# Performance work log

Hardware: AMD Instinct MI355X
Metric: run time of the kernel (lower is better)

The kernel has to match this reference:

```python
import jax, jax.numpy as jnp
import numpy as np

B, T, D = 4, 2048, 1024
H = 16
HD = D // H  # 64
SCALE = 1.0 / np.sqrt(HD).astype(np.float32)


def setup_inputs() -> dict:
    key = jax.random.key(0)
    ks = jax.random.split(key, 5)
    std = 0.02
    return {
        "x": jax.random.normal(ks[0], (B, T, D), dtype=jnp.float32),
        "wq": jax.random.normal(ks[1], (D, D), dtype=jnp.float32) * std,
        "wk": jax.random.normal(ks[2], (D, D), dtype=jnp.float32) * std,
        "wv": jax.random.normal(ks[3], (D, D), dtype=jnp.float32) * std,
        "wo": jax.random.normal(ks[4], (D, D), dtype=jnp.float32) * std,
    }


def _shape(t):
    # [B,T,D] -> [B,H,T,HD]
    Bt, Tt, _ = t.shape
    return t.reshape(Bt, Tt, H, HD).transpose(0, 2, 1, 3)


def reference(x, wq, wk, wv, wo):
    # Linear layers are y = x @ W^T (torch nn.Linear semantics, no bias)
    q = _shape(x @ wq.T)  # [B,H,T,HD]
    k = _shape(x @ wk.T)
    v = _shape(x @ wv.T)
    att = jnp.einsum("bhqd,bhkd->bhqk", q, k) * SCALE  # [B,H,T,T]
    # causal mask: -inf strictly above diagonal
    causal = jnp.triu(jnp.full((T, T), -jnp.inf, dtype=att.dtype), k=1)
    att = att + causal[None, None, :, :]
    att = jax.nn.softmax(att.astype(jnp.float32), axis=-1).astype(att.dtype)
    # dropout prob = 0.0 -> identity
    y = jnp.einsum("bhqk,bhkd->bhqd", att, v)  # [B,H,T,HD]
    y = y.transpose(0, 2, 1, 3).reshape(B, T, D)
    return y @ wo.T
```

## Files before the change

kernel.cpp:

```cpp
#include <hip/hip_runtime.h>
#include <hip/hip_bf16.h>

#define BB 4
#define TT 2048
#define DDIM 1024
#define HH 16
#define HD 64

typedef __bf16 bf16_t;
typedef __bf16 bf16x4 __attribute__((ext_vector_type(4)));
typedef __bf16 bf16x8 __attribute__((ext_vector_type(8)));
typedef float f32x4 __attribute__((ext_vector_type(4)));

#define GLOAD_LDS(gp, lp) \
    __builtin_amdgcn_global_load_lds( \
        (const __attribute__((address_space(1))) void*)(gp), \
        (__attribute__((address_space(3))) void*)(lp), 16, 0, 0)

__global__ __launch_bounds__(256) void cvt_f32_bf16(
    const float* __restrict__ src, bf16_t* __restrict__ dst, size_t n8)
{
    size_t i = (size_t)blockIdx.x * blockDim.x + threadIdx.x;
    const size_t stride = (size_t)gridDim.x * blockDim.x;
    for (; i < n8; i += stride) {
        const f32x4 a = ((const f32x4*)src)[2 * i];
        const f32x4 b = ((const f32x4*)src)[2 * i + 1];
        bf16x8 v;
#pragma unroll
        for (int j = 0; j < 4; j++) { v[j] = (bf16_t)a[j]; v[4 + j] = (bf16_t)b[j]; }
        ((bf16x8*)dst)[i] = v;
    }
}

__global__ __launch_bounds__(256) void cvt_wpack(
    const float* __restrict__ s0, const float* __restrict__ s1,
    const float* __restrict__ s2, const float* __restrict__ s3,
    bf16_t* __restrict__ dst)
{
    const size_t n8 = (size_t)4 * DDIM * DDIM / 8;
    size_t i = (size_t)blockIdx.x * blockDim.x + threadIdx.x;
    const size_t stride = (size_t)gridDim.x * blockDim.x;
    for (; i < n8; i += stride) {
        const int sel = (int)(i >> 17);
        const float* s = sel == 0 ? s0 : sel == 1 ? s1 : sel == 2 ? s2 : s3;
        const size_t off8 = i & ((1u << 17) - 1);
        const f32x4 a = ((const f32x4*)s)[2 * off8];
        const f32x4 b = ((const f32x4*)s)[2 * off8 + 1];
        bf16x8 v;
#pragma unroll
        for (int j = 0; j < 4; j++) { v[j] = (bf16_t)a[j]; v[4 + j] = (bf16_t)b[j]; }
        ((bf16x8*)dst)[i] = v;
    }
}

__device__ __forceinline__ void stage8(const bf16_t* __restrict__ g, int ld,
                                       bf16_t* __restrict__ ldsbase, int lane)
{
    const int rr = lane >> 3;
    const int cc = (lane & 7) ^ ((rr & 1) << 2);
    GLOAD_LDS(&g[(size_t)rr * ld + cc * 8], ldsbase);
}

__global__ __launch_bounds__(256) void gemm_qkv(
    const bf16_t* __restrict__ A, const bf16_t* __restrict__ Wqkv,
    bf16_t* __restrict__ Qo, bf16_t* __restrict__ Ko, bf16_t* __restrict__ Vto,
    int M, int K)
{
    __shared__ alignas(16) bf16_t As[128 * 64];
    __shared__ alignas(16) bf16_t Bs[128 * 64];

    const int tid  = threadIdx.x;
    const int lane = tid & 63;
    const int w    = tid >> 6;
    const int quad = lane >> 4;
    const int l15  = lane & 15;
    const int wm   = (w >> 1) * 64;
    const int wn   = (w & 1) * 64;

    const int nwg = gridDim.x * gridDim.y;
    const int cpx = nwg >> 3;
    int id = blockIdx.y * gridDim.x + blockIdx.x;
    id = (id & 7) * cpx + (id >> 3);
    const int tileN = (id % 24) * 128;
    const int tileM = (id / 24) * 128;

    const f32x4 vzero = {0.f, 0.f, 0.f, 0.f};
    f32x4 acc[4][4];
#pragma unroll
    for (int i = 0; i < 4; i++)
#pragma unroll
        for (int j = 0; j < 4; j++) acc[i][j] = vzero;

    const int par4 = (l15 & 1) << 2;

    for (int k0 = 0; k0 < K; k0 += 64) {
        __syncthreads();
#pragma unroll
        for (int q = 0; q < 4; q++) {
            const int r0 = w * 32 + q * 8;
            stage8(&A[(size_t)(tileM + r0) * K + k0], K, &As[r0 * 64], lane);
            stage8(&Wqkv[(size_t)(tileN + r0) * K + k0], K, &Bs[r0 * 64], lane);
        }
        __syncthreads();

#pragma unroll
        for (int ss = 0; ss < 2; ss++) {
            const int phys = ((ss * 4 + quad) ^ par4) << 3;
            bf16x8 af[4], bf[4];
#pragma unroll
            for (int i = 0; i < 4; i++)
                af[i] = *(bf16x8*)&As[(wm + i * 16 + l15) * 64 + phys];
#pragma unroll
            for (int j = 0; j < 4; j++)
                bf[j] = *(bf16x8*)&Bs[(wn + j * 16 + l15) * 64 + phys];
#pragma unroll
            for (int i = 0; i < 4; i++)
#pragma unroll
                for (int j = 0; j < 4; j++)
                    acc[i][j] = __builtin_amdgcn_mfma_f32_16x16x32_bf16(
                        af[i], bf[j], acc[i][j], 0, 0, 0);
        }
    }

    const int region = tileN >> 10;
    const float osc = (region == 0) ? 0.125f * 1.44269504f : 1.0f;
#pragma unroll
    for (int i = 0; i < 4; i++) {
        const int row = tileM + wm + i * 16 + quad * 4;
#pragma unroll
        for (int j = 0; j < 4; j++) {
            const int ncol = tileN + wn + j * 16 + l15;
            if (region == 2) {
                const int cl = ncol - 2048;
                const int h = cl >> 6, d = cl & 63;
                const int bb = row >> 11, tloc = row & (TT - 1);
                bf16x4 pk;
#pragma unroll
                for (int r = 0; r < 4; r++) pk[r] = (bf16_t)acc[i][j][r];
                *(bf16x4*)&Vto[(((size_t)bb * HH + h) * HD + d) * TT + tloc] = pk;
            } else {
                bf16_t* dst = (region == 0) ? Qo : Ko;
                const int cl = ncol & 1023;
#pragma unroll
                for (int r = 0; r < 4; r++)
                    dst[(size_t)(row + r) * DDIM + cl] = (bf16_t)(acc[i][j][r] * osc);
            }
        }
    }
}

__global__ __launch_bounds__(256) void gemm_out(
    const bf16_t* __restrict__ A, const bf16_t* __restrict__ Bm,
    float* __restrict__ C, int M, int N, int K)
{
    __shared__ alignas(16) bf16_t As[128 * 64];
    __shared__ alignas(16) bf16_t Bs[128 * 64];

    const int tid  = threadIdx.x;
    const int lane = tid & 63;
    const int w    = tid >> 6;
    const int quad = lane >> 4;
    const int l15  = lane & 15;
    const int wm   = (w >> 1) * 64;
    const int wn   = (w & 1) * 64;

    const int nwg = gridDim.x * gridDim.y;
    const int cpx = nwg >> 3;
    int id = blockIdx.y * gridDim.x + blockIdx.x;
    id = (id & 7) * cpx + (id >> 3);
    const int tileN = (id % 8) * 128;
    const int tileM = (id / 8) * 128;

    const f32x4 vzero = {0.f, 0.f, 0.f, 0.f};
    f32x4 acc[4][4];
#pragma unroll
    for (int i = 0; i < 4; i++)
#pragma unroll
        for (int j = 0; j < 4; j++) acc[i][j] = vzero;

    const int par4 = (l15 & 1) << 2;

    for (int k0 = 0; k0 < K; k0 += 64) {
        __syncthreads();
#pragma unroll
        for (int q = 0; q < 4; q++) {
            const int r0 = w * 32 + q * 8;
            stage8(&A[(size_t)(tileM + r0) * K + k0], K, &As[r0 * 64], lane);
            stage8(&Bm[(size_t)(tileN + r0) * K + k0], K, &Bs[r0 * 64], lane);
        }
        __syncthreads();

#pragma unroll
        for (int ss = 0; ss < 2; ss++) {
            const int phys = ((ss * 4 + quad) ^ par4) << 3;
            bf16x8 af[4], bf[4];
#pragma unroll
            for (int i = 0; i < 4; i++)
                af[i] = *(bf16x8*)&As[(wm + i * 16 + l15) * 64 + phys];
#pragma unroll
            for (int j = 0; j < 4; j++)
                bf[j] = *(bf16x8*)&Bs[(wn + j * 16 + l15) * 64 + phys];
#pragma unroll
            for (int i = 0; i < 4; i++)
#pragma unroll
                for (int j = 0; j < 4; j++)
                    acc[i][j] = __builtin_amdgcn_mfma_f32_16x16x32_bf16(
                        af[i], bf[j], acc[i][j], 0, 0, 0);
        }
    }

#pragma unroll
    for (int i = 0; i < 4; i++) {
#pragma unroll
        for (int r = 0; r < 4; r++) {
            const int row = tileM + wm + i * 16 + quad * 4 + r;
#pragma unroll
            for (int j = 0; j < 4; j++)
                C[(size_t)row * N + tileN + wn + j * 16 + l15] = acc[i][j][r];
        }
    }
}

__global__ __launch_bounds__(256, 2) void attn_causal(
    const bf16_t* __restrict__ Q, const bf16_t* __restrict__ Kg,
    const bf16_t* __restrict__ Vt_g, bf16_t* __restrict__ Y)
{
    __shared__ alignas(16) bf16_t Ks[2 * 64 * 72];
    __shared__ alignas(16) bf16_t Vt[2 * 64 * 72];
    __shared__ alignas(16) bf16_t Ps[4][32 * 72];

    const int tid  = threadIdx.x;
    const int lane = tid & 63;
    const int w    = tid >> 6;
    const int quad = lane >> 4;
    const int l15  = lane & 15;
    const int bh   = blockIdx.x;
    const int sp   = blockIdx.y;
    const int b = bh >> 4, h = bh & 15;

    const int stg_row = tid >> 3;
    const int stg_c8  = (tid & 7) * 8;
    const int stg_off = stg_row * 72 + stg_c8;

    const f32x4 vzero = {0.f, 0.f, 0.f, 0.f};
    bf16x8 ones;
#pragma unroll
    for (int j = 0; j < 8; j++) ones[j] = (l15 == 0) ? (bf16_t)1.0f : (bf16_t)0.0f;

    const bf16_t* kg0 = &Kg[(size_t)(b * TT + stg_row) * DDIM + h * 64 + stg_c8];
    const bf16_t* vg0 = &Vt_g[((size_t)bh * HD + stg_row) * TT + stg_c8];

#pragma unroll 1
    for (int half = 0; half < 2; half++) {
        const int strip = half ? (15 - sp) : sp;
        const int qbase = strip * 128;

        bf16x8 qf[2][2];
#pragma unroll
        for (int mi = 0; mi < 2; mi++) {
            const size_t rq =
                (size_t)(b * TT + qbase + w * 32 + mi * 16 + l15) * DDIM + h * 64;
            qf[mi][0] = *(const bf16x8*)&Q[rq + quad * 8];
            qf[mi][1] = *(const bf16x8*)&Q[rq + 32 + quad * 8];
        }

        f32x4 o[2][4], o4[2];
#pragma unroll
        for (int mi = 0; mi < 2; mi++) {
#pragma unroll
            for (int c = 0; c < 4; c++) o[mi][c] = vzero;
            o4[mi] = vzero;
        }

        const int nkt = 2 * strip + 2;

        bf16x8 kreg[2], vreg[2];
#pragma unroll
        for (int p = 0; p < 2; p++) {
            kreg[p] = *(const bf16x8*)&kg0[(size_t)(p * 32) * DDIM];
            vreg[p] = *(const bf16x8*)&vg0[(size_t)(p * 32) * TT];
        }

#pragma unroll 1
        for (int kt = 0; kt < nkt; kt++) {
            const int kbase = kt * 64;
            const int coff = (kt & 1) * (64 * 72);
#pragma unroll
            for (int p = 0; p < 2; p++) {
                *(bf16x8*)&Ks[coff + stg_off + p * 32 * 72] = kreg[p];
                *(bf16x8*)&Vt[coff + stg_off + p * 32 * 72] = vreg[p];
            }
            if (kt + 1 < nkt) {
                const int nb = (kt + 1) * 64;
#pragma unroll
                for (int p = 0; p < 2; p++) {
                    kreg[p] = *(const bf16x8*)&kg0[(size_t)(nb + p * 32) * DDIM];
                    vreg[p] = *(const bf16x8*)&vg0[(size_t)(p * 32) * TT + nb];
                }
            }
            __syncthreads();

            f32x4 s[2][4];
            __builtin_amdgcn_s_setprio(1);
#pragma unroll
            for (int c = 0; c < 4; c++) {
                bf16x8 kf0 = *(bf16x8*)&Ks[coff + (c * 16 + l15) * 72 + quad * 8];
                bf16x8 kf1 = *(bf16x8*)&Ks[coff + (c * 16 + l15) * 72 + 32 + quad * 8];
#pragma unroll
                for (int mi = 0; mi < 2; mi++) {
                    f32x4 t = __builtin_amdgcn_mfma_f32_16x16x32_bf16(
                        qf[mi][0], kf0, vzero, 0, 0, 0);
                    s[mi][c] = __builtin_amdgcn_mfma_f32_16x16x32_bf16(
                        qf[mi][1], kf1, t, 0, 0, 0);
                }
            }
            __builtin_amdgcn_s_setprio(0);

#pragma unroll
            for (int mi = 0; mi < 2; mi++) {
                const int qlow = qbase + w * 32 + mi * 16;
                const bool need = (kbase + 63 > qlow);
#pragma unroll
                for (int r = 0; r < 4; r++) {
                    const int qrow = qlow + quad * 4 + r;
                    const int prow = mi * 16 + quad * 4 + r;
#pragma unroll
                    for (int c = 0; c < 4; c++) {
                        float sv = s[mi][c][r];
                        if (need && (kbase + c * 16 + l15 > qrow)) sv = -1e30f;
                        const int pchunk = (c * 2 + (l15 >> 3)) ^ (prow >> 2);
                        Ps[w][prow * 72 + (pchunk << 3) + (l15 & 7)] =
                            (bf16_t)__builtin_amdgcn_exp2f(sv);
                    }
                }
            }

            __builtin_amdgcn_s_setprio(1);
#pragma unroll
            for (int ss = 0; ss < 2; ss++) {
                bf16x8 pf[2];
#pragma unroll
                for (int mi = 0; mi < 2; mi++) {
                    const int m = mi * 16 + l15;
                    pf[mi] = *(bf16x8*)&Ps[w][m * 72 +
                                              ((((ss * 4 + quad) ^ (m >> 2)) & 7) << 3)];
                }
#pragma unroll
                for (int c = 0; c < 4; c++) {
                    bf16x8 vf = *(bf16x8*)&Vt[coff + (c * 16 + l15) * 72 + ss * 32 + quad * 8];
#pragma unroll
                    for (int mi = 0; mi < 2; mi++)
                        o[mi][c] = __builtin_amdgcn_mfma_f32_16x16x32_bf16(
                            pf[mi], vf, o[mi][c], 0, 0, 0);
                }
#pragma unroll
                for (int mi = 0; mi < 2; mi++)
                    o4[mi] = __builtin_amdgcn_mfma_f32_16x16x32_bf16(
                        pf[mi], ones, o4[mi], 0, 0, 0);
            }
            __builtin_amdgcn_s_setprio(0);
        }

#pragma unroll
        for (int mi = 0; mi < 2; mi++) {
#pragma unroll
            for (int r = 0; r < 4; r++) {
                const float lsum = __shfl(o4[mi][r], lane & 48, 64);
                const float inv = 1.0f / lsum;
                const int q = qbase + w * 32 + mi * 16 + quad * 4 + r;
#pragma unroll
                for (int c = 0; c < 4; c++)
                    Y[(size_t)(b * TT + q) * DDIM + h * 64 + c * 16 + l15] =
                        (bf16_t)(o[mi][c][r] * inv);
            }
        }
    }
}

extern "C" void kernel_launch(void* const* d_in, const int* in_sizes, int n_in,
                              void* d_out, int out_size, void* d_ws, size_t ws_size,
                              hipStream_t stream) {
    (void)in_sizes; (void)n_in; (void)out_size;
    const float* x  = (const float*)d_in[0];
    float* out = (float*)d_out;

    const int M = BB * TT;
    const size_t REGION = (size_t)M * DDIM;
    const size_t WREG   = (size_t)DDIM * DDIM;
    const size_t BATCH  = (size_t)TT * DDIM;
    bf16_t* ws = (bf16_t*)d_ws;

    if (ws_size >= (72ull << 20)) {
        bf16_t* xb  = ws;
        bf16_t* wpk = ws + REGION;
        bf16_t* Qb  = wpk + 4 * WREG;
        bf16_t* Kb  = Qb + REGION;
        bf16_t* Vtb = Kb + REGION;

        cvt_f32_bf16<<<1024, 256, 0, stream>>>(x, xb, REGION / 8);
        cvt_wpack<<<512, 256, 0, stream>>>(
            (const float*)d_in[1], (const float*)d_in[2],
            (const float*)d_in[3], (const float*)d_in[4], wpk);

        gemm_qkv<<<dim3(24, M / 128), 256, 0, stream>>>(
            xb, wpk, Qb, Kb, Vtb, M, DDIM);
        attn_causal<<<dim3(BB * HH, 8), 256, 0, stream>>>(Qb, Kb, Vtb, Qb);
        gemm_out<<<dim3(8, M / 128), 256, 0, stream>>>(
            Qb, wpk + 3 * WREG, out, M, DDIM, DDIM);
    } else {
        bf16_t* wpk = ws;
        bf16_t* xbb = ws + 4 * WREG;
        bf16_t* Qb  = xbb + BATCH;
        bf16_t* Kb  = Qb + BATCH;
        bf16_t* Vtb = Kb + BATCH;

        cvt_wpack<<<512, 256, 0, stream>>>(
            (const float*)d_in[1], (const float*)d_in[2],
            (const float*)d_in[3], (const float*)d_in[4], wpk);

        for (int b = 0; b < BB; b++) {
            const float* x_b = x + (size_t)b * BATCH;
            float* out_b = out + (size_t)b * BATCH;
            cvt_f32_bf16<<<512, 256, 0, stream>>>(x_b, xbb, BATCH / 8);
            gemm_qkv<<<dim3(24, TT / 128), 256, 0, stream>>>(
                xbb, wpk, Qb, Kb, Vtb, TT, DDIM);
            attn_causal<<<dim3(HH, 8), 256, 0, stream>>>(Qb, Kb, Vtb, Qb);
            gemm_out<<<dim3(8, TT / 128), 256, 0, stream>>>(
                Qb, wpk + 3 * WREG, out_b, TT, DDIM, DDIM);
        }
    }
}
```

Before: 254.4 us.

## Double-buffer GEMM LDS tiles, widen XOR swizzle, and raise attention occupancy

Both projection GEMMs now use two LDS buffers, so the next K-tile's global-to-LDS copy is issued before the MFMAs on the current tile, with one barrier per iteration instead of two. MFMA blocks are wrapped in raised wave priority. The LDS swizzle changes from a 1-bit XOR to a full 3-bit row XOR in the GEMMs and in attention, where the padded 72-wide K/V tiles become unpadded 64-wide swizzled tiles. The saved LDS lets attention's launch bound ask for 3 blocks per CU, at the cost of register pressure and the GEMMs' doubled LDS footprint.

Result: faster. 244.8 us (-3.8%).

```diff
diff --git a/kernel.cpp b/kernel.cpp
--- a/kernel.cpp
+++ b/kernel.cpp
@@ -57,7 +57,7 @@
                                        bf16_t* __restrict__ ldsbase, int lane)
 {
     const int rr = lane >> 3;
-    const int cc = (lane & 7) ^ ((rr & 1) << 2);
+    const int cc = (lane & 7) ^ rr;
     GLOAD_LDS(&g[(size_t)rr * ld + cc * 8], ldsbase);
 }
 
@@ -66,8 +66,8 @@
     bf16_t* __restrict__ Qo, bf16_t* __restrict__ Ko, bf16_t* __restrict__ Vto,
     int M, int K)
 {
-    __shared__ alignas(16) bf16_t As[128 * 64];
-    __shared__ alignas(16) bf16_t Bs[128 * 64];
+    __shared__ alignas(16) bf16_t As[2][128 * 64];
+    __shared__ alignas(16) bf16_t Bs[2][128 * 64];
 
     const int tid  = threadIdx.x;
     const int lane = tid & 63;
@@ -91,35 +91,51 @@
 #pragma unroll
         for (int j = 0; j < 4; j++) acc[i][j] = vzero;
 
-    const int par4 = (l15 & 1) << 2;
-
-    for (int k0 = 0; k0 < K; k0 += 64) {
-        __syncthreads();
-#pragma unroll
-        for (int q = 0; q < 4; q++) {
-            const int r0 = w * 32 + q * 8;
-            stage8(&A[(size_t)(tileM + r0) * K + k0], K, &As[r0 * 64], lane);
-            stage8(&Wqkv[(size_t)(tileN + r0) * K + k0], K, &Bs[r0 * 64], lane);
-        }
-        __syncthreads();
+    const int par8 = l15 & 7;
+
+#pragma unroll
+    for (int q = 0; q < 4; q++) {
+        const int r0 = w * 32 + q * 8;
+        stage8(&A[(size_t)(tileM + r0) * K], K, &As[0][r0 * 64], lane);
+        stage8(&Wqkv[(size_t)(tileN + r0) * K], K, &Bs[0][r0 * 64], lane);
+    }
+    __syncthreads();
+
+    const int NT = K >> 6;
+    for (int t = 0; t < NT; ++t) {
+        const int cur = t & 1;
+        if (t + 1 < NT) {
+            const int k0 = (t + 1) << 6;
+#pragma unroll
+            for (int q = 0; q < 4; q++) {
+                const int r0 = w * 32 + q * 8;
+                stage8(&A[(size_t)(tileM + r0) * K + k0], K,
+                       &As[cur ^ 1][r0 * 64], lane);
+                stage8(&Wqkv[(size_t)(tileN + r0) * K + k0], K,
+                       &Bs[cur ^ 1][r0 * 64], lane);
+            }
+        }
 
 #pragma unroll
         for (int ss = 0; ss < 2; ss++) {
-            const int phys = ((ss * 4 + quad) ^ par4) << 3;
+            const int phys = ((ss * 4 + quad) ^ par8) << 3;
             bf16x8 af[4], bf[4];
 #pragma unroll
             for (int i = 0; i < 4; i++)
-                af[i] = *(bf16x8*)&As[(wm + i * 16 + l15) * 64 + phys];
+                af[i] = *(bf16x8*)&As[cur][(wm + i * 16 + l15) * 64 + phys];
 #pragma unroll
             for (int j = 0; j < 4; j++)
-                bf[j] = *(bf16x8*)&Bs[(wn + j * 16 + l15) * 64 + phys];
+                bf[j] = *(bf16x8*)&Bs[cur][(wn + j * 16 + l15) * 64 + phys];
+            __builtin_amdgcn_s_setprio(1);
 #pragma unroll
             for (int i = 0; i < 4; i++)
 #pragma unroll
                 for (int j = 0; j < 4; j++)
                     acc[i][j] = __builtin_amdgcn_mfma_f32_16x16x32_bf16(
                         af[i], bf[j], acc[i][j], 0, 0, 0);
-        }
+            __builtin_amdgcn_s_setprio(0);
+        }
+        __syncthreads();
     }
 
     const int region = tileN >> 10;
@@ -153,8 +169,8 @@
     const bf16_t* __restrict__ A, const bf16_t* __restrict__ Bm,
     float* __restrict__ C, int M, int N, int K)
 {
-    __shared__ alignas(16) bf16_t As[128 * 64];
-    __shared__ alignas(16) bf16_t Bs[128 * 64];
+    __shared__ alignas(16) bf16_t As[2][128 * 64];
+    __shared__ alignas(16) bf16_t Bs[2][128 * 64];
 
     const int tid  = threadIdx.x;
     const int lane = tid & 63;
@@ -178,35 +194,51 @@
 #pragma unroll
         for (int j = 0; j < 4; j++) acc[i][j] = vzero;
 
-    const int par4 = (l15 & 1) << 2;
-
-    for (int k0 = 0; k0 < K; k0 += 64) {
-        __syncthreads();
-#pragma unroll
-        for (int q = 0; q < 4; q++) {
-            const int r0 = w * 32 + q * 8;
-            stage8(&A[(size_t)(tileM + r0) * K + k0], K, &As[r0 * 64], lane);
-            stage8(&Bm[(size_t)(tileN + r0) * K + k0], K, &Bs[r0 * 64], lane);
-        }
-        __syncthreads();
+    const int par8 = l15 & 7;
+
+#pragma unroll
+    for (int q = 0; q < 4; q++) {
+        const int r0 = w * 32 + q * 8;
+        stage8(&A[(size_t)(tileM + r0) * K], K, &As[0][r0 * 64], lane);
+        stage8(&Bm[(size_t)(tileN + r0) * K], K, &Bs[0][r0 * 64], lane);
+    }
+    __syncthreads();
+
+    const int NT = K >> 6;
+    for (int t = 0; t < NT; ++t) {
+        const int cur = t & 1;
+        if (t + 1 < NT) {
+            const int k0 = (t + 1) << 6;
+#pragma unroll
+            for (int q = 0; q < 4; q++) {
+                const int r0 = w * 32 + q * 8;
+                stage8(&A[(size_t)(tileM + r0) * K + k0], K,
+                       &As[cur ^ 1][r0 * 64], lane);
+                stage8(&Bm[(size_t)(tileN + r0) * K + k0], K,
+                       &Bs[cur ^ 1][r0 * 64], lane);
+            }
+        }
 
 #pragma unroll
         for (int ss = 0; ss < 2; ss++) {
-            const int phys = ((ss * 4 + quad) ^ par4) << 3;
+            const int phys = ((ss * 4 + quad) ^ par8) << 3;
             bf16x8 af[4], bf[4];
 #pragma unroll
             for (int i = 0; i < 4; i++)
-                af[i] = *(bf16x8*)&As[(wm + i * 16 + l15) * 64 + phys];
+                af[i] = *(bf16x8*)&As[cur][(wm + i * 16 + l15) * 64 + phys];
 #pragma unroll
             for (int j = 0; j < 4; j++)
-                bf[j] = *(bf16x8*)&Bs[(wn + j * 16 + l15) * 64 + phys];
+                bf[j] = *(bf16x8*)&Bs[cur][(wn + j * 16 + l15) * 64 + phys];
+            __builtin_amdgcn_s_setprio(1);
 #pragma unroll
             for (int i = 0; i < 4; i++)
 #pragma unroll
                 for (int j = 0; j < 4; j++)
                     acc[i][j] = __builtin_amdgcn_mfma_f32_16x16x32_bf16(
                         af[i], bf[j], acc[i][j], 0, 0, 0);
-        }
+            __builtin_amdgcn_s_setprio(0);
+        }
+        __syncthreads();
     }
 
 #pragma unroll
@@ -221,12 +253,12 @@
     }
 }
 
-__global__ __launch_bounds__(256, 2) void attn_causal(
+__global__ __launch_bounds__(256, 3) void attn_causal(
     const bf16_t* __restrict__ Q, const bf16_t* __restrict__ Kg,
     const bf16_t* __restrict__ Vt_g, bf16_t* __restrict__ Y)
 {
-    __shared__ alignas(16) bf16_t Ks[2 * 64 * 72];
-    __shared__ alignas(16) bf16_t Vt[2 * 64 * 72];
+    __shared__ alignas(16) bf16_t Ks[2 * 64 * 64];
+    __shared__ alignas(16) bf16_t Vt[2 * 64 * 64];
     __shared__ alignas(16) bf16_t Ps[4][32 * 72];
 
     const int tid  = threadIdx.x;
@@ -240,7 +272,8 @@
 
     const int stg_row = tid >> 3;
     const int stg_c8  = (tid & 7) * 8;
-    const int stg_off = stg_row * 72 + stg_c8;
+    const int stg_off = stg_row * 64 + ((((tid & 7) ^ (stg_row & 7))) << 3);
+    const int par8 = l15 & 7;
 
     const f32x4 vzero = {0.f, 0.f, 0.f, 0.f};
     bf16x8 ones;
@@ -284,11 +317,11 @@
 #pragma unroll 1
         for (int kt = 0; kt < nkt; kt++) {
             const int kbase = kt * 64;
-            const int coff = (kt & 1) * (64 * 72);
+            const int coff = (kt & 1) * (64 * 64);
 #pragma unroll
             for (int p = 0; p < 2; p++) {
-                *(bf16x8*)&Ks[coff + stg_off + p * 32 * 72] = kreg[p];
-                *(bf16x8*)&Vt[coff + stg_off + p * 32 * 72] = vreg[p];
+                *(bf16x8*)&Ks[coff + stg_off + p * 32 * 64] = kreg[p];
+                *(bf16x8*)&Vt[coff + stg_off + p * 32 * 64] = vreg[p];
             }
             if (kt + 1 < nkt) {
                 const int nb = (kt + 1) * 64;
@@ -304,8 +337,9 @@
             __builtin_amdgcn_s_setprio(1);
 #pragma unroll
             for (int c = 0; c < 4; c++) {
-                bf16x8 kf0 = *(bf16x8*)&Ks[coff + (c * 16 + l15) * 72 + quad * 8];
-                bf16x8 kf1 = *(bf16x8*)&Ks[coff + (c * 16 + l15) * 72 + 32 + quad * 8];
+                const int krow = (c * 16 + l15) * 64;
+                bf16x8 kf0 = *(bf16x8*)&Ks[coff + krow + ((quad ^ par8) << 3)];
+                bf16x8 kf1 = *(bf16x8*)&Ks[coff + krow + (((4 + quad) ^ par8) << 3)];
 #pragma unroll
                 for (int mi = 0; mi < 2; mi++) {
                     f32x4 t = __builtin_amdgcn_mfma_f32_16x16x32_bf16(
@@ -347,7 +381,8 @@
                 }
 #pragma unroll
                 for (int c = 0; c < 4; c++) {
-                    bf16x8 vf = *(bf16x8*)&Vt[coff + (c * 16 + l15) * 72 + ss * 32 + quad * 8];
+                    bf16x8 vf = *(bf16x8*)&Vt[coff + (c * 16 + l15) * 64 +
+                                              (((ss * 4 + quad) ^ par8) << 3)];
 #pragma unroll
                     for (int mi = 0; mi < 2; mi++)
                         o[mi][c] = __builtin_amdgcn_mfma_f32_16x16x32_bf16(
```
